# Optimization experiments

Measured on AMD Instinct MI355X. Metric: run time of the kernel, lower is better.

Reference implementation:

```python
import jax, jax.numpy as jnp
import numpy as np

B, T, D, U = 32, 2048, 1024, 1024


def setup_inputs() -> dict:
    key = jax.random.key(0)
    ks = jax.random.split(key, 6)
    scale = 0.02
    return {
        "query": jax.random.normal(ks[0], (B, D), jnp.float32),
        "values": jax.random.normal(ks[1], (B, T, D), jnp.float32),
        "W1_k": jax.random.normal(ks[2], (D, U), jnp.float32) * scale,
        "W1_b": jnp.zeros((U,), jnp.float32),
        "W2_k": jax.random.normal(ks[3], (D, U), jnp.float32) * scale,
        "W2_b": jnp.zeros((U,), jnp.float32),
        "V_k": jax.random.normal(ks[4], (U, 1), jnp.float32) * scale,
        "V_b": jnp.zeros((1,), jnp.float32),
    }


def reference(query, values, W1_k, W1_b, W2_k, W2_b, V_k, V_b):
    # query: [B, D] -> [B, 1, U]; values: [B, T, D] -> [B, T, U]
    q_proj = (query @ W1_k + W1_b)[:, None, :]
    v_proj = jnp.einsum("btd,du->btu", values, W2_k) + W2_b
    # score: [B, T, 1]
    score = jnp.tanh(q_proj + v_proj) @ V_k + V_b
    attention_weights = jax.nn.softmax(score, axis=1)  # over time axis T
    context_vector = jnp.sum(attention_weights * values, axis=1)  # [B, D]
    return context_vector
```

## Files before the change

kernel.cpp:

```cpp
#include <hip/hip_runtime.h>

#define NB 32
#define NT 2048
#define ND 1024
#define NU 1024
#define NM (NB*NT)

using f32x4 = __attribute__((ext_vector_type(4))) float;
using s16x8 = __attribute__((ext_vector_type(8))) short;

#define BAR()   asm volatile("s_barrier" ::: "memory")
#define LGKM0() asm volatile("s_waitcnt lgkmcnt(0)" ::: "memory")
#define VMC(n)  asm volatile("s_waitcnt vmcnt(" #n ")" ::: "memory")

__device__ __forceinline__ unsigned short f2bf(float f) {
  unsigned u = __builtin_bit_cast(unsigned, f);
  u = u + 0x7fffu + ((u >> 16) & 1u);
  return (unsigned short)(u >> 16);
}

__device__ __forceinline__ unsigned cvtpk(float lo, float hi) {
  unsigned r;
  asm("v_cvt_pk_bf16_f32 %0, %1, %2" : "=v"(r) : "v"(lo), "v"(hi));
  return r;
}

__device__ __forceinline__ void gload_lds16(const void* g, void* l) {
  __builtin_amdgcn_global_load_lds(
      (const __attribute__((address_space(1))) unsigned int*)g,
      (__attribute__((address_space(3))) unsigned int*)l, 16, 0, 0);
}

__device__ __forceinline__ float tanh_fast(float x) {
  float e = __expf(2.0f * x);
  return 1.0f - 2.0f * __builtin_amdgcn_rcpf(e + 1.0f);
}

__device__ __forceinline__ void stage_half(const unsigned short* g, int gk,
                                           unsigned short* l, int w, int r3, int c8s) {
#pragma unroll
  for (int i = 0; i < 2; ++i) {
    int cb = i * 8 + w;
    gload_lds16(g + (((size_t)(cb * 8 + r3)) << 10) + gk + c8s * 8, l + cb * 512);
  }
}

__device__ __forceinline__ void load_halfA(const float* g, int kbase, int arow, int acol,
                                           float4 (&f)[4]) {
  const float* p = g + ((size_t)arow << 10) + kbase + acol * 16;
  f[0] = *(const float4*)(p);
  f[1] = *(const float4*)(p + 4);
  f[2] = *(const float4*)(p + 8);
  f[3] = *(const float4*)(p + 12);
}

__device__ __forceinline__ void cvt_half(const float4 (&f)[4], unsigned (&pk)[8]) {
  pk[0] = cvtpk(f[0].x, f[0].y); pk[1] = cvtpk(f[0].z, f[0].w);
  pk[2] = cvtpk(f[1].x, f[1].y); pk[3] = cvtpk(f[1].z, f[1].w);
  pk[4] = cvtpk(f[2].x, f[2].y); pk[5] = cvtpk(f[2].z, f[2].w);
  pk[6] = cvtpk(f[3].x, f[3].y); pk[7] = cvtpk(f[3].z, f[3].w);
}

__device__ __forceinline__ void write_half(const unsigned (&pk)[8], unsigned short* lds,
                                           int row, int acol) {
  int r7 = row & 7;
  int c0 = (acol * 2) ^ r7, c1 = (acol * 2 + 1) ^ r7;
  *(uint4*)(lds + (row << 6) + c0 * 8) = make_uint4(pk[0], pk[1], pk[2], pk[3]);
  *(uint4*)(lds + (row << 6) + c1 * 8) = make_uint4(pk[4], pk[5], pk[6], pk[7]);
}

#define MFMA_Q(MB, NBASE) \
  _Pragma("unroll") \
  for (int m = 0; m < 4; ++m) { \
    _Pragma("unroll") \
    for (int n = 0; n < 2; ++n) { \
      _Pragma("unroll") \
      for (int ks = 0; ks < 2; ++ks) \
        acc[(MB) + m][(NBASE) + n] = __builtin_amdgcn_mfma_f32_16x16x32_bf16( \
            fa[m][ks], fb[n][ks], acc[(MB) + m][(NBASE) + n], 0, 0, 0); \
    } \
  }

template<bool AISS, bool BST>
__device__ __forceinline__ void tile_body(
    int kt, int buf, const float* gA, const unsigned short* gB,
    unsigned short* sA, unsigned short* sB, f32x4 (&acc)[8][4],
    int w, int wr, int wc, int l15, int lg, int r3, int c8s, int arow, int acol) {
  const unsigned short* pA = sA + buf * 16384;
  const unsigned short* pB = sB + buf * 16384;
  unsigned short* nA = sA + buf * 16384;
  unsigned short* nB = sB + (buf ^ 1) * 16384;
  const int l7 = l15 & 7;
  s16x8 fa[4][2], fb[2][2];
  float4 ah[4];
  unsigned pk0[8], pk1[8];
  VMC(0);
#pragma unroll
  for (int m = 0; m < 4; ++m)
#pragma unroll
    for (int ks = 0; ks < 2; ++ks)
      fa[m][ks] = *(const s16x8*)(pA + ((wr * 128 + m * 16 + l15) << 6) + (((ks * 4 + lg) ^ l7) << 3));
#pragma unroll
  for (int n = 0; n < 2; ++n)
#pragma unroll
    for (int ks = 0; ks < 2; ++ks)
      fb[n][ks] = *(const s16x8*)(pB + ((wc * 64 + n * 16 + l15) << 6) + (((ks * 4 + lg) ^ l7) << 3));
  if (AISS) load_halfA(gA, (kt + 2) * 64, arow, acol, ah);
  BAR(); LGKM0(); __builtin_amdgcn_sched_barrier(0);
  __builtin_amdgcn_s_setprio(1); MFMA_Q(0, 0); __builtin_amdgcn_s_setprio(0);
  BAR();
#pragma unroll
  for (int n = 0; n < 2; ++n)
#pragma unroll
    for (int ks = 0; ks < 2; ++ks)
      fb[n][ks] = *(const s16x8*)(pB + ((wc * 64 + (2 + n) * 16 + l15) << 6) + (((ks * 4 + lg) ^ l7) << 3));
  if (BST) stage_half(gB, (kt + 1) * 64, nB, w, r3, c8s);
  BAR(); LGKM0(); __builtin_amdgcn_sched_barrier(0);
  __builtin_amdgcn_s_setprio(1); MFMA_Q(0, 2); __builtin_amdgcn_s_setprio(0);
  BAR();
#pragma unroll
  for (int m = 0; m < 4; ++m)
#pragma unroll
    for (int ks = 0; ks < 2; ++ks)
      fa[m][ks] = *(const s16x8*)(pA + ((wr * 128 + (4 + m) * 16 + l15) << 6) + (((ks * 4 + lg) ^ l7) << 3));
  if (AISS) {
    VMC(2);
    cvt_half(ah, pk0);
    load_halfA(gA + (128 << 10), (kt + 2) * 64, arow, acol, ah);
  }
  if (BST) stage_half(gB + (128 << 10), (kt + 1) * 64, nB + 8192, w, r3, c8s);
  BAR(); LGKM0(); __builtin_amdgcn_sched_barrier(0);
  __builtin_amdgcn_s_setprio(1); MFMA_Q(4, 2); __builtin_amdgcn_s_setprio(0);
  BAR();
#pragma unroll
  for (int n = 0; n < 2; ++n)
#pragma unroll
    for (int ks = 0; ks < 2; ++ks)
      fb[n][ks] = *(const s16x8*)(pB + ((wc * 64 + n * 16 + l15) << 6) + (((ks * 4 + lg) ^ l7) << 3));
  if (AISS) {
    VMC(2);
    cvt_half(ah, pk1);
  }
  LGKM0(); __builtin_amdgcn_sched_barrier(0);
  __builtin_amdgcn_s_setprio(1); MFMA_Q(4, 0); __builtin_amdgcn_s_setprio(0);
  if (AISS) {
    write_half(pk0, nA, arow, acol);
    write_half(pk1, nA, 128 + arow, acol);
  }
  BAR();
}

__global__ __launch_bounds__(512, 2) void k_score_gemm8(
    const float* __restrict__ values, const unsigned short* __restrict__ W2t,
    const float* __restrict__ add2, const float* __restrict__ Vk,
    float* __restrict__ score_part) {
  __shared__ unsigned short sA[32768];
  __shared__ unsigned short sB[32768];
  const int tid = threadIdx.x;
  const int w = tid >> 6, lane = tid & 63;
  const int wr = w >> 2, wc = w & 3;
  const int l15 = lane & 15, lg = lane >> 4;
  const int r3 = lane >> 3, c8s = (lane & 7) ^ r3;
  const int arow = tid >> 2, acol = tid & 3;

  const int L = blockIdx.x;
  const int g = (L & 7) * 128 + (L >> 3);
  const int mtile = g >> 2, ntile = g & 3;

  const float* gA = values + ((size_t)mtile << 18);
  const unsigned short* gB = W2t + ((size_t)ntile << 18);

  f32x4 acc[8][4] = {};

  {
    float4 f0[4], f1[4];
    unsigned p0[8], p1[8];
    load_halfA(gA, 0, arow, acol, f0);
    load_halfA(gA + (128 << 10), 0, arow, acol, f1);
    VMC(0);
    cvt_half(f0, p0); cvt_half(f1, p1);
    write_half(p0, sA, arow, acol);
    write_half(p1, sA, 128 + arow, acol);
    load_halfA(gA, 64, arow, acol, f0);
    load_halfA(gA + (128 << 10), 64, arow, acol, f1);
    stage_half(gB, 0, sB, w, r3, c8s);
    stage_half(gB + (128 << 10), 0, sB + 8192, w, r3, c8s);
    VMC(4);
    cvt_half(f0, p0); cvt_half(f1, p1);
    write_half(p0, sA + 16384, arow, acol);
    write_half(p1, sA + 16384, 128 + arow, acol);
    VMC(0);
    LGKM0();
    BAR();
  }

  int buf = 0;
  for (int kt = 0; kt < 14; ++kt) {
    tile_body<true, true>(kt, buf, gA, gB, sA, sB, acc, w, wr, wc, l15, lg, r3, c8s, arow, acol);
    buf ^= 1;
  }
  tile_body<false, true>(14, buf, gA, gB, sA, sB, acc, w, wr, wc, l15, lg, r3, c8s, arow, acol);
  buf ^= 1;
  tile_body<false, false>(15, buf, gA, gB, sA, sB, acc, w, wr, wc, l15, lg, r3, c8s, arow, acol);

  const int b = (mtile * 256) >> 11;
  float vks[4], adds[4];
#pragma unroll
  for (int n = 0; n < 4; ++n) {
    int u = ntile * 256 + wc * 64 + n * 16 + l15;
    vks[n] = Vk[u];
    adds[n] = add2[(b << 10) + u];
  }
  __syncthreads();
  float* part = (float*)sA;
#pragma unroll
  for (int m = 0; m < 8; ++m) {
#pragma unroll
    for (int j = 0; j < 4; ++j) {
      float s = 0.f;
#pragma unroll
      for (int n = 0; n < 4; ++n) {
        float x = acc[m][n][j] + adds[n];
        s = fmaf(tanh_fast(x), vks[n], s);
      }
#pragma unroll
      for (int off = 1; off < 16; off <<= 1) s += __shfl_xor(s, off);
      if (l15 == 0) part[wc * 256 + wr * 128 + m * 16 + lg * 4 + j] = s;
    }
  }
  __syncthreads();
  if (tid < 256) {
    float v = part[tid] + part[256 + tid] + part[512 + tid] + part[768 + tid];
    score_part[((size_t)ntile << 16) + mtile * 256 + tid] = v;
  }
}

__global__ void k_qproj(const float* __restrict__ q, const float* __restrict__ W1,
                        const float* __restrict__ W1b, const float* __restrict__ W2b,
                        float* __restrict__ add2) {
  int u = blockIdx.x * 256 + threadIdx.x;
  int b = blockIdx.y;
  const float* qr = q + (b << 10);
  float s = 0.f;
#pragma unroll 8
  for (int d = 0; d < ND; ++d) s = fmaf(qr[d], W1[d * NU + u], s);
  add2[(b << 10) + u] = s + W1b[u] + W2b[u];
}

__global__ void k_w2t(const float* __restrict__ W2, unsigned short* __restrict__ W2t) {
  __shared__ unsigned short tile[64][65];
  int bu = blockIdx.x * 64, bd = blockIdx.y * 64;
  int x = threadIdx.x & 63, y4 = threadIdx.x >> 6;
#pragma unroll
  for (int r = 0; r < 16; ++r) {
    int dl = y4 * 16 + r;
    tile[x][dl] = f2bf(W2[(size_t)(bd + dl) * NU + bu + x]);
  }
  __syncthreads();
#pragma unroll
  for (int r = 0; r < 16; ++r) {
    int ul = y4 * 16 + r;
    W2t[(size_t)(bu + ul) * ND + bd + x] = tile[ul][x];
  }
}

__global__ void k_softmax(const float* __restrict__ sp, float* __restrict__ w) {
  __shared__ float redm[4], reds[4];
  int b = blockIdx.x, tid = threadIdx.x;
  float s[8];
  float mx = -1e30f;
#pragma unroll
  for (int i = 0; i < 8; ++i) {
    int t = i * 256 + tid;
    float v = 0.f;
#pragma unroll
    for (int p = 0; p < 4; ++p) v += sp[((size_t)p << 16) + (b << 11) + t];
    s[i] = v;
    mx = fmaxf(mx, v);
  }
#pragma unroll
  for (int o = 1; o < 64; o <<= 1) mx = fmaxf(mx, __shfl_xor(mx, o));
  if ((tid & 63) == 0) redm[tid >> 6] = mx;
  __syncthreads();
  mx = fmaxf(fmaxf(redm[0], redm[1]), fmaxf(redm[2], redm[3]));
  float sum = 0.f;
#pragma unroll
  for (int i = 0; i < 8; ++i) { s[i] = __expf(s[i] - mx); sum += s[i]; }
#pragma unroll
  for (int o = 1; o < 64; o <<= 1) sum += __shfl_xor(sum, o);
  if ((tid & 63) == 0) reds[tid >> 6] = sum;
  __syncthreads();
  float inv = 1.0f / (reds[0] + reds[1] + reds[2] + reds[3]);
#pragma unroll
  for (int i = 0; i < 8; ++i) w[(b << 11) + i * 256 + tid] = s[i] * inv;
}

__global__ void k_context(const float* __restrict__ values, const float* __restrict__ wv,
                          float* __restrict__ part) {
  int d4 = threadIdx.x;
  int b = blockIdx.y, tc = blockIdx.z;
  const float4* vb = (const float4*)(values + ((size_t)b << 21) + ((size_t)tc << 18)) + d4;
  const float* wb = wv + (b << 11) + (tc << 8);
  float ax = 0.f, ay = 0.f, az = 0.f, aw = 0.f;
#pragma unroll 4
  for (int t = 0; t < 256; ++t) {
    float4 v = vb[(size_t)t << 8];
    float wt = wb[t];
    ax = fmaf(wt, v.x, ax); ay = fmaf(wt, v.y, ay);
    az = fmaf(wt, v.z, az); aw = fmaf(wt, v.w, aw);
  }
  float4* po = (float4*)(part + (((size_t)tc * NB + b) << 10)) + d4;
  *po = make_float4(ax, ay, az, aw);
}

__global__ void k_ctx_reduce(const float* __restrict__ part, float* __restrict__ out) {
  int i = blockIdx.x * 256 + threadIdx.x;
  float s = 0.f;
#pragma unroll
  for (int p = 0; p < 8; ++p) s += part[(p << 15) + i];
  out[i] = s;
}

extern "C" void kernel_launch(void* const* d_in, const int* in_sizes, int n_in,
                              void* d_out, int out_size, void* d_ws, size_t ws_size,
                              hipStream_t stream) {
  const float* query  = (const float*)d_in[0];
  const float* values = (const float*)d_in[1];
  const float* W1k    = (const float*)d_in[2];
  const float* W1b    = (const float*)d_in[3];
  const float* W2k    = (const float*)d_in[4];
  const float* W2b    = (const float*)d_in[5];
  const float* Vk     = (const float*)d_in[6];
  float* out = (float*)d_out;
  char* ws = (char*)d_ws;

  size_t off = 0;
  float* add2 = (float*)(ws + off); off += (size_t)NB * NU * 4;
  float* sp   = (float*)(ws + off); off += (size_t)4 * NM * 4;
  float* wv   = (float*)(ws + off); off += (size_t)NM * 4;
  float* ctxp = (float*)(ws + off); off += (size_t)8 * NB * ND * 4;
  unsigned short* W2t = (unsigned short*)(ws + off); off += (size_t)NU * ND * 2;

  k_qproj<<<dim3(4, 32), 256, 0, stream>>>(query, W1k, W1b, W2b, add2);
  k_w2t<<<dim3(16, 16), 256, 0, stream>>>(W2k, W2t);
  k_score_gemm8<<<dim3(1024), 512, 0, stream>>>(values, W2t, add2, Vk, sp);
  k_softmax<<<dim3(32), 256, 0, stream>>>(sp, wv);
  k_context<<<dim3(1, 32, 8), 256, 0, stream>>>(values, wv, ctxp);
  k_ctx_reduce<<<dim3(128), 256, 0, stream>>>(ctxp, out);
}
```

Before: 323.2 us.

## Restructure GEMM pipeline: prefetch B two tiles ahead, keep A in registers

Reworks the per-tile software pipeline of the score GEMM. B tiles are now staged via LDS DMA two k-steps ahead into the buffer just consumed. Raw fp32 A values are held in registers across iterations and converted and written into the other LDS buffer mid-tile. All four B fragments load up front, removing one fragment-reload phase, several barriers and the full vmcnt(0) wait at the start of each tile. The goal is to hide global latency better and cut synchronization stalls, at the cost of more live registers and reliance on implicit waits for the DMA-staged B data, which could be a correctness risk.

```diff
diff --git a/kernel.cpp b/kernel.cpp
--- a/kernel.cpp
+++ b/kernel.cpp
@@ -12,6 +12,7 @@
 #define BAR()   asm volatile("s_barrier" ::: "memory")
 #define LGKM0() asm volatile("s_waitcnt lgkmcnt(0)" ::: "memory")
 #define VMC(n)  asm volatile("s_waitcnt vmcnt(" #n ")" ::: "memory")
+#define SB0()   __builtin_amdgcn_sched_barrier(0)
 
 __device__ __forceinline__ unsigned short f2bf(float f) {
   unsigned u = __builtin_bit_cast(unsigned, f);
@@ -69,84 +70,68 @@
   *(uint4*)(lds + (row << 6) + c1 * 8) = make_uint4(pk[4], pk[5], pk[6], pk[7]);
 }
 
-#define MFMA_Q(MB, NBASE) \
+#define MFMA_Q(MB, NB2) \
   _Pragma("unroll") \
   for (int m = 0; m < 4; ++m) { \
     _Pragma("unroll") \
     for (int n = 0; n < 2; ++n) { \
       _Pragma("unroll") \
       for (int ks = 0; ks < 2; ++ks) \
-        acc[(MB) + m][(NBASE) + n] = __builtin_amdgcn_mfma_f32_16x16x32_bf16( \
-            fa[m][ks], fb[n][ks], acc[(MB) + m][(NBASE) + n], 0, 0, 0); \
+        acc[(MB) + m][(NB2) + n] = __builtin_amdgcn_mfma_f32_16x16x32_bf16( \
+            fa[m][ks], fb[(NB2) + n][ks], acc[(MB) + m][(NB2) + n], 0, 0, 0); \
     } \
   }
 
-template<bool AISS, bool BST>
+template<bool ACVT, bool AISS, bool BST>
 __device__ __forceinline__ void tile_body(
     int kt, int buf, const float* gA, const unsigned short* gB,
-    unsigned short* sA, unsigned short* sB, f32x4 (&acc)[8][4],
+    unsigned short* sA, unsigned short* sB, f32x4 (&acc)[8][4], float4 (&ah)[2][4],
     int w, int wr, int wc, int l15, int lg, int r3, int c8s, int arow, int acol) {
   const unsigned short* pA = sA + buf * 16384;
   const unsigned short* pB = sB + buf * 16384;
-  unsigned short* nA = sA + buf * 16384;
-  unsigned short* nB = sB + (buf ^ 1) * 16384;
+  unsigned short* wA = sA + (buf ^ 1) * 16384;
+  unsigned short* nB = sB + buf * 16384;
   const int l7 = l15 & 7;
-  s16x8 fa[4][2], fb[2][2];
-  float4 ah[4];
-  unsigned pk0[8], pk1[8];
-  VMC(0);
+  s16x8 fa[4][2], fb[4][2];
 #pragma unroll
   for (int m = 0; m < 4; ++m)
 #pragma unroll
     for (int ks = 0; ks < 2; ++ks)
       fa[m][ks] = *(const s16x8*)(pA + ((wr * 128 + m * 16 + l15) << 6) + (((ks * 4 + lg) ^ l7) << 3));
 #pragma unroll
-  for (int n = 0; n < 2; ++n)
+  for (int n = 0; n < 4; ++n)
 #pragma unroll
     for (int ks = 0; ks < 2; ++ks)
       fb[n][ks] = *(const s16x8*)(pB + ((wc * 64 + n * 16 + l15) << 6) + (((ks * 4 + lg) ^ l7) << 3));
-  if (AISS) load_halfA(gA, (kt + 2) * 64, arow, acol, ah);
-  BAR(); LGKM0(); __builtin_amdgcn_sched_barrier(0);
+  BAR(); LGKM0(); SB0();
   __builtin_amdgcn_s_setprio(1); MFMA_Q(0, 0); __builtin_amdgcn_s_setprio(0);
   BAR();
-#pragma unroll
-  for (int n = 0; n < 2; ++n)
-#pragma unroll
-    for (int ks = 0; ks < 2; ++ks)
-      fb[n][ks] = *(const s16x8*)(pB + ((wc * 64 + (2 + n) * 16 + l15) << 6) + (((ks * 4 + lg) ^ l7) << 3));
-  if (BST) stage_half(gB, (kt + 1) * 64, nB, w, r3, c8s);
-  BAR(); LGKM0(); __builtin_amdgcn_sched_barrier(0);
+  if (ACVT) {
+    unsigned pk[8];
+    cvt_half(ah[0], pk);
+    write_half(pk, wA, arow, acol);
+  }
+  if (BST) stage_half(gB, (kt + 2) * 64, nB, w, r3, c8s);
   __builtin_amdgcn_s_setprio(1); MFMA_Q(0, 2); __builtin_amdgcn_s_setprio(0);
+  LGKM0();
   BAR();
 #pragma unroll
   for (int m = 0; m < 4; ++m)
 #pragma unroll
     for (int ks = 0; ks < 2; ++ks)
       fa[m][ks] = *(const s16x8*)(pA + ((wr * 128 + (4 + m) * 16 + l15) << 6) + (((ks * 4 + lg) ^ l7) << 3));
-  if (AISS) {
-    VMC(2);
-    cvt_half(ah, pk0);
-    load_halfA(gA + (128 << 10), (kt + 2) * 64, arow, acol, ah);
-  }
-  if (BST) stage_half(gB + (128 << 10), (kt + 1) * 64, nB + 8192, w, r3, c8s);
-  BAR(); LGKM0(); __builtin_amdgcn_sched_barrier(0);
+  if (ACVT) {
+    unsigned pk[8];
+    cvt_half(ah[1], pk);
+    write_half(pk, wA, 128 + arow, acol);
+  }
+  if (AISS) load_halfA(gA, (kt + 2) * 64, arow, acol, ah[0]);
+  if (BST) stage_half(gB + (128 << 10), (kt + 2) * 64, nB + 8192, w, r3, c8s);
+  LGKM0(); SB0();
+  __builtin_amdgcn_s_setprio(1); MFMA_Q(4, 0); __builtin_amdgcn_s_setprio(0);
+  BAR();
+  if (AISS) load_halfA(gA + (128 << 10), (kt + 2) * 64, arow, acol, ah[1]);
   __builtin_amdgcn_s_setprio(1); MFMA_Q(4, 2); __builtin_amdgcn_s_setprio(0);
-  BAR();
-#pragma unroll
-  for (int n = 0; n < 2; ++n)
-#pragma unroll
-    for (int ks = 0; ks < 2; ++ks)
-      fb[n][ks] = *(const s16x8*)(pB + ((wc * 64 + n * 16 + l15) << 6) + (((ks * 4 + lg) ^ l7) << 3));
-  if (AISS) {
-    VMC(2);
-    cvt_half(ah, pk1);
-  }
-  LGKM0(); __builtin_amdgcn_sched_barrier(0);
-  __builtin_amdgcn_s_setprio(1); MFMA_Q(4, 0); __builtin_amdgcn_s_setprio(0);
-  if (AISS) {
-    write_half(pk0, nA, arow, acol);
-    write_half(pk1, nA, 128 + arow, acol);
-  }
   BAR();
 }
 
@@ -171,37 +156,35 @@
   const unsigned short* gB = W2t + ((size_t)ntile << 18);
 
   f32x4 acc[8][4] = {};
+  float4 ah[2][4];
 
   {
     float4 f0[4], f1[4];
     unsigned p0[8], p1[8];
     load_halfA(gA, 0, arow, acol, f0);
     load_halfA(gA + (128 << 10), 0, arow, acol, f1);
-    VMC(0);
     cvt_half(f0, p0); cvt_half(f1, p1);
     write_half(p0, sA, arow, acol);
     write_half(p1, sA, 128 + arow, acol);
-    load_halfA(gA, 64, arow, acol, f0);
-    load_halfA(gA + (128 << 10), 64, arow, acol, f1);
     stage_half(gB, 0, sB, w, r3, c8s);
     stage_half(gB + (128 << 10), 0, sB + 8192, w, r3, c8s);
-    VMC(4);
-    cvt_half(f0, p0); cvt_half(f1, p1);
-    write_half(p0, sA + 16384, arow, acol);
-    write_half(p1, sA + 16384, 128 + arow, acol);
-    VMC(0);
+    stage_half(gB, 64, sB + 16384, w, r3, c8s);
+    stage_half(gB + (128 << 10), 64, sB + 16384 + 8192, w, r3, c8s);
+    load_halfA(gA, 64, arow, acol, ah[0]);
+    load_halfA(gA + (128 << 10), 64, arow, acol, ah[1]);
+    VMC(8);
     LGKM0();
     BAR();
   }
 
   int buf = 0;
   for (int kt = 0; kt < 14; ++kt) {
-    tile_body<true, true>(kt, buf, gA, gB, sA, sB, acc, w, wr, wc, l15, lg, r3, c8s, arow, acol);
+    tile_body<true, true, true>(kt, buf, gA, gB, sA, sB, acc, ah, w, wr, wc, l15, lg, r3, c8s, arow, acol);
     buf ^= 1;
   }
-  tile_body<false, true>(14, buf, gA, gB, sA, sB, acc, w, wr, wc, l15, lg, r3, c8s, arow, acol);
+  tile_body<true, false, false>(14, buf, gA, gB, sA, sB, acc, ah, w, wr, wc, l15, lg, r3, c8s, arow, acol);
   buf ^= 1;
-  tile_body<false, false>(15, buf, gA, gB, sA, sB, acc, w, wr, wc, l15, lg, r3, c8s, arow, acol);
+  tile_body<false, false, false>(15, buf, gA, gB, sA, sB, acc, ah, w, wr, wc, l15, lg, r3, c8s, arow, acol);
 
   const int b = (mtile * 256) >> 11;
   float vks[4], adds[4];
```

Result: faster. 298.2 us (-7.7%).
